# Performance work log

Measured on AMD Instinct MI355X. Metric: run time of the kernel, lower is better.

## Reference

```python
import jax, jax.numpy as jnp
import numpy as np

B, N, D = 16, 2048, 64

def setup_inputs() -> dict:
    key = jax.random.key(0)
    kq, kk, kv = jax.random.split(key, 3)
    q = jax.random.normal(kq, (B, N, D), dtype=jnp.float32)
    k = jax.random.normal(kk, (B, N, D), dtype=jnp.float32)
    v = jax.random.normal(kv, (B, N, D), dtype=jnp.float32)
    scale = jnp.float32(1.0 / np.sqrt(D))  # canonical 1/sqrt(d_head)
    return {"q": q, "k": k, "v": v, "scale": scale}

def reference(q, k, v, scale):
    # attention = softmax((q @ k^T) * scale) over key axis; dropout p=0.0 is identity
    scores = jnp.einsum('bqd,bkd->bqk', q, k) * scale  # [B,N,N]
    attention = jax.nn.softmax(scores, axis=2)
    context = jnp.einsum('bqk,bkd->bqd', attention, v)  # [B,N,D]
    return (context, attention)
```

## Files before the change

### kernel.cpp

```cpp
#include <hip/hip_runtime.h>

#define Bb 16
#define Nn 2048
#define Dd 64

typedef __attribute__((ext_vector_type(8))) short s16x8;
typedef __attribute__((ext_vector_type(4))) short s16x4;
typedef __attribute__((ext_vector_type(4))) float fx4;

__device__ __forceinline__ unsigned short f2bf(float f) {
  union { float f; unsigned u; } v; v.f = f;
  unsigned r = v.u + 0x7FFFu + ((v.u >> 16) & 1u);
  return (unsigned short)(r >> 16);
}

__global__ void k_cvtK(const float* __restrict__ K, unsigned short* __restrict__ Kb) {
  int i = blockIdx.x * 256 + threadIdx.x;
  float4 f = ((const float4*)K)[i];
  ushort4 o;
  o.x = f2bf(f.x); o.y = f2bf(f.y); o.z = f2bf(f.z); o.w = f2bf(f.w);
  ((ushort4*)Kb)[i] = o;
}

__global__ void k_transV(const float* __restrict__ V, unsigned short* __restrict__ VT) {
  __shared__ float tile[32][33];
  int b = blockIdx.z;
  int j0 = blockIdx.x * 32, d0 = blockIdx.y * 32;
  int tx = threadIdx.x, ty = threadIdx.y;
  const float* Vb = V + (size_t)b * Nn * Dd;
  unsigned short* Tb = VT + (size_t)b * Dd * Nn;
  for (int r = ty; r < 32; r += 8)
    tile[r][tx] = Vb[(size_t)(j0 + r) * Dd + d0 + tx];
  __syncthreads();
  for (int r = ty; r < 32; r += 8)
    Tb[(size_t)(d0 + r) * Nn + j0 + tx] = f2bf(tile[tx][r]);
}

__global__ __launch_bounds__(256) void k_attn(
    const float* __restrict__ Q, const unsigned short* __restrict__ Kbf,
    const unsigned short* __restrict__ VTbf, const float* __restrict__ scale_p,
    float* __restrict__ ctx, float* att) {
  const int id = blockIdx.x;
  const int swz = ((id & 7) << 8) | (id >> 3);
  const int b = swz >> 7;
  const int q0 = (swz & 127) << 4;

  const int tid = threadIdx.x;
  const int wave = tid >> 6, lane = tid & 63;
  const int nl = lane & 15, quad = lane >> 4;
  const int qrow = q0 + nl;
  const float c2 = scale_p[0] * 1.44269504088896341f;

  __shared__ float sm[4][16];
  __shared__ float sl[4][16];
  __shared__ float ob[4][16][64];

  s16x8 qb[2];
  {
    const float* qp = Q + ((size_t)b * Nn + qrow) * Dd + quad * 8;
#pragma unroll
    for (int kt = 0; kt < 2; ++kt) {
      float4 f0 = *(const float4*)(qp + kt * 32);
      float4 f1 = *(const float4*)(qp + kt * 32 + 4);
      s16x8 t;
      t[0] = (short)f2bf(f0.x); t[1] = (short)f2bf(f0.y);
      t[2] = (short)f2bf(f0.z); t[3] = (short)f2bf(f0.w);
      t[4] = (short)f2bf(f1.x); t[5] = (short)f2bf(f1.y);
      t[6] = (short)f2bf(f1.z); t[7] = (short)f2bf(f1.w);
      qb[kt] = t;
    }
  }
  const unsigned short* Kb = Kbf + (size_t)b * Nn * Dd;
  const unsigned short* VTb = VTbf + (size_t)b * Dd * Nn;
  float* attb = att + (size_t)b * Nn * Nn;

  float m = -3.0e38f, l = 0.0f;

  for (int t = 0; t < 4; ++t) {
    const int k0 = (wave * 4 + t) * 128;
    fx4 s[8];
#pragma unroll
    for (int nt = 0; nt < 8; ++nt) s[nt] = (fx4){0.f, 0.f, 0.f, 0.f};
#pragma unroll
    for (int nt = 0; nt < 8; ++nt) {
      const s16x8* ka =
          (const s16x8*)(Kb + ((size_t)(k0 + nt * 16 + nl)) * Dd + quad * 8);
      s[nt] = __builtin_amdgcn_mfma_f32_16x16x32_bf16(ka[0], qb[0], s[nt], 0, 0, 0);
      s[nt] = __builtin_amdgcn_mfma_f32_16x16x32_bf16(ka[4], qb[1], s[nt], 0, 0, 0);
    }
    float lm = s[0][0];
#pragma unroll
    for (int nt = 0; nt < 8; ++nt)
#pragma unroll
      for (int r = 0; r < 4; ++r) lm = fmaxf(lm, s[nt][r]);
    float mn = fmaxf(m, lm * c2);
    float ls = 0.f;
#pragma unroll
    for (int nt = 0; nt < 8; ++nt)
#pragma unroll
      for (int r = 0; r < 4; ++r) ls += exp2f(fmaf(s[nt][r], c2, -mn));
    l = l * exp2f(m - mn) + ls;
    m = mn;
  }
#pragma unroll
  for (int mask = 16; mask <= 32; mask <<= 1) {
    float om = __shfl_xor(m, mask, 64);
    float ol = __shfl_xor(l, mask, 64);
    float mn = fmaxf(m, om);
    l = l * exp2f(m - mn) + ol * exp2f(om - mn);
    m = mn;
  }
  if (lane < 16) { sm[wave][lane] = m; sl[wave][lane] = l; }
  __syncthreads();
  float rinv;
  {
    float M = sm[0][nl], L = sl[0][nl];
#pragma unroll
    for (int j = 1; j < 4; ++j) {
      float mj = sm[j][nl], lj = sl[j][nl];
      float mn = fmaxf(M, mj);
      L = L * exp2f(M - mn) + lj * exp2f(mj - mn);
      M = mn;
    }
    m = M;
    rinv = 1.0f / L;
  }

  fx4 o[4];
#pragma unroll
  for (int d = 0; d < 4; ++d) o[d] = (fx4){0.f, 0.f, 0.f, 0.f};

  for (int t = 0; t < 4; ++t) {
    const int k0 = (wave * 4 + t) * 128;
    fx4 s[8];
#pragma unroll
    for (int nt = 0; nt < 8; ++nt) s[nt] = (fx4){0.f, 0.f, 0.f, 0.f};
#pragma unroll
    for (int nt = 0; nt < 8; ++nt) {
      const s16x8* ka =
          (const s16x8*)(Kb + ((size_t)(k0 + nt * 16 + nl)) * Dd + quad * 8);
      s[nt] = __builtin_amdgcn_mfma_f32_16x16x32_bf16(ka[0], qb[0], s[nt], 0, 0, 0);
      s[nt] = __builtin_amdgcn_mfma_f32_16x16x32_bf16(ka[4], qb[1], s[nt], 0, 0, 0);
    }
#pragma unroll
    for (int nt = 0; nt < 8; ++nt) {
      s16x4 vb[4];
#pragma unroll
      for (int ntd = 0; ntd < 4; ++ntd)
        vb[ntd] = *(const s16x4*)(VTb + ((size_t)(ntd * 16 + nl)) * Nn + k0 +
                                  nt * 16 + quad * 4);
      fx4 p;
#pragma unroll
      for (int r = 0; r < 4; ++r)
        p[r] = exp2f(fmaf(s[nt][r], c2, -m)) * rinv;
      *(fx4*)(attb + (size_t)qrow * Nn + k0 + nt * 16 + quad * 4) = p;
      s16x4 pa;
      pa[0] = (short)f2bf(p[0]); pa[1] = (short)f2bf(p[1]);
      pa[2] = (short)f2bf(p[2]); pa[3] = (short)f2bf(p[3]);
#pragma unroll
      for (int ntd = 0; ntd < 4; ++ntd)
        o[ntd] = __builtin_amdgcn_mfma_f32_16x16x16bf16_1k(pa, vb[ntd], o[ntd], 0, 0, 0);
    }
  }

#pragma unroll
  for (int ntd = 0; ntd < 4; ++ntd)
#pragma unroll
    for (int r = 0; r < 4; ++r)
      ob[wave][quad * 4 + r][ntd * 16 + nl] = o[ntd][r];
  __syncthreads();
  {
    const int row = tid >> 4;
    const int col = (tid & 15) << 2;
    fx4 a = *(const fx4*)&ob[0][row][col];
#pragma unroll
    for (int j = 1; j < 4; ++j) {
      fx4 tt = *(const fx4*)&ob[j][row][col];
      a[0] += tt[0]; a[1] += tt[1]; a[2] += tt[2]; a[3] += tt[3];
    }
    *(fx4*)(ctx + ((size_t)b * Nn + q0 + row) * Dd + col) = a;
  }
}

extern "C" void kernel_launch(void* const* d_in, const int* in_sizes, int n_in,
                              void* d_out, int out_size, void* d_ws, size_t ws_size,
                              hipStream_t stream) {
  const float* q = (const float*)d_in[0];
  const float* k = (const float*)d_in[1];
  const float* v = (const float*)d_in[2];
  const float* scale = (const float*)d_in[3];

  float* ctx = (float*)d_out;
  float* att = ctx + (size_t)Bb * Nn * Dd;

  unsigned short* Kbf = (unsigned short*)d_ws;
  unsigned short* VTbf = Kbf + (size_t)Bb * Nn * Dd;

  hipLaunchKernelGGL(k_cvtK, dim3((Bb * Nn * Dd) / (256 * 4)), dim3(256), 0, stream,
                     k, Kbf);
  hipLaunchKernelGGL(k_transV, dim3(Nn / 32, Dd / 32, Bb), dim3(32, 8), 0, stream,
                     v, VTbf);
  hipLaunchKernelGGL(k_attn, dim3(Bb * Nn / 16), dim3(256), 0, stream,
                     q, Kbf, VTbf, scale, ctx, att);
}
```

Before: 493.1 us.

## Stage attention tiles in swizzled LDS for coalesced nontemporal stores; split reductions

The attention probabilities were written straight from the MFMA register layout, so each lane stored 16 bytes at scattered rows. Each wave now stages 16x64 tiles in a per-wave, XOR-swizzled shared buffer and writes whole row segments with nontemporal stores, which should improve coalescing and cut cache pollution on the dominant 268MB output. The row max and sum reductions are also split into four independent chains to shorten dependency latency. This adds LDS traffic and relies on an lgkmcnt wait rather than a barrier within each wave.

```diff
diff --git a/kernel.cpp b/kernel.cpp
--- a/kernel.cpp
+++ b/kernel.cpp
@@ -53,7 +53,7 @@
 
   __shared__ float sm[4][16];
   __shared__ float sl[4][16];
-  __shared__ float ob[4][16][64];
+  __shared__ float obf[4 * 1024];
 
   s16x8 qb[2];
   {
@@ -88,17 +88,23 @@
       s[nt] = __builtin_amdgcn_mfma_f32_16x16x32_bf16(ka[0], qb[0], s[nt], 0, 0, 0);
       s[nt] = __builtin_amdgcn_mfma_f32_16x16x32_bf16(ka[4], qb[1], s[nt], 0, 0, 0);
     }
-    float lm = s[0][0];
-#pragma unroll
-    for (int nt = 0; nt < 8; ++nt)
-#pragma unroll
-      for (int r = 0; r < 4; ++r) lm = fmaxf(lm, s[nt][r]);
+    float x0 = s[0][0], x1 = s[0][1], x2 = s[0][2], x3 = s[0][3];
+#pragma unroll
+    for (int nt = 1; nt < 8; ++nt) {
+      x0 = fmaxf(x0, s[nt][0]); x1 = fmaxf(x1, s[nt][1]);
+      x2 = fmaxf(x2, s[nt][2]); x3 = fmaxf(x3, s[nt][3]);
+    }
+    float lm = fmaxf(fmaxf(x0, x1), fmaxf(x2, x3));
     float mn = fmaxf(m, lm * c2);
-    float ls = 0.f;
-#pragma unroll
-    for (int nt = 0; nt < 8; ++nt)
-#pragma unroll
-      for (int r = 0; r < 4; ++r) ls += exp2f(fmaf(s[nt][r], c2, -mn));
+    float a0 = 0.f, a1 = 0.f, a2 = 0.f, a3 = 0.f;
+#pragma unroll
+    for (int nt = 0; nt < 8; ++nt) {
+      a0 += exp2f(fmaf(s[nt][0], c2, -mn));
+      a1 += exp2f(fmaf(s[nt][1], c2, -mn));
+      a2 += exp2f(fmaf(s[nt][2], c2, -mn));
+      a3 += exp2f(fmaf(s[nt][3], c2, -mn));
+    }
+    float ls = (a0 + a1) + (a2 + a3);
     l = l * exp2f(m - mn) + ls;
     m = mn;
   }
@@ -130,6 +136,8 @@
 #pragma unroll
   for (int d = 0; d < 4; ++d) o[d] = (fx4){0.f, 0.f, 0.f, 0.f};
 
+  float* myob = obf + wave * 1024;
+
   for (int t = 0; t < 4; ++t) {
     const int k0 = (wave * 4 + t) * 128;
     fx4 s[8];
@@ -143,42 +151,66 @@
       s[nt] = __builtin_amdgcn_mfma_f32_16x16x32_bf16(ka[4], qb[1], s[nt], 0, 0, 0);
     }
 #pragma unroll
-    for (int nt = 0; nt < 8; ++nt) {
-      s16x4 vb[4];
-#pragma unroll
-      for (int ntd = 0; ntd < 4; ++ntd)
-        vb[ntd] = *(const s16x4*)(VTb + ((size_t)(ntd * 16 + nl)) * Nn + k0 +
-                                  nt * 16 + quad * 4);
-      fx4 p;
-#pragma unroll
-      for (int r = 0; r < 4; ++r)
-        p[r] = exp2f(fmaf(s[nt][r], c2, -m)) * rinv;
-      *(fx4*)(attb + (size_t)qrow * Nn + k0 + nt * 16 + quad * 4) = p;
-      s16x4 pa;
-      pa[0] = (short)f2bf(p[0]); pa[1] = (short)f2bf(p[1]);
-      pa[2] = (short)f2bf(p[2]); pa[3] = (short)f2bf(p[3]);
-#pragma unroll
-      for (int ntd = 0; ntd < 4; ++ntd)
-        o[ntd] = __builtin_amdgcn_mfma_f32_16x16x16bf16_1k(pa, vb[ntd], o[ntd], 0, 0, 0);
+    for (int c = 0; c < 2; ++c) {
+#pragma unroll
+      for (int n4 = 0; n4 < 4; ++n4) {
+        const int nt = c * 4 + n4;
+        s16x4 vb[4];
+#pragma unroll
+        for (int ntd = 0; ntd < 4; ++ntd)
+          vb[ntd] = *(const s16x4*)(VTb + ((size_t)(ntd * 16 + nl)) * Nn + k0 +
+                                    nt * 16 + quad * 4);
+        fx4 p;
+#pragma unroll
+        for (int r = 0; r < 4; ++r)
+          p[r] = exp2f(fmaf(s[nt][r], c2, -m)) * rinv;
+        {
+          const int su = (n4 * 4 + quad) ^ (nl & 7);
+          *(fx4*)&myob[nl * 64 + su * 4] = p;
+        }
+        s16x4 pa;
+        pa[0] = (short)f2bf(p[0]); pa[1] = (short)f2bf(p[1]);
+        pa[2] = (short)f2bf(p[2]); pa[3] = (short)f2bf(p[3]);
+#pragma unroll
+        for (int ntd = 0; ntd < 4; ++ntd)
+          o[ntd] = __builtin_amdgcn_mfma_f32_16x16x16bf16_1k(pa, vb[ntd], o[ntd], 0, 0, 0);
+      }
+      asm volatile("s_waitcnt lgkmcnt(0)" ::: "memory");
+      {
+        const int rl = lane >> 4, un = lane & 15;
+#pragma unroll
+        for (int rb = 0; rb < 4; ++rb) {
+          const int row = rb * 4 + rl;
+          const int su = un ^ (row & 7);
+          fx4 val = *(const fx4*)&myob[row * 64 + su * 4];
+          __builtin_nontemporal_store(
+              val, (fx4*)(attb + (size_t)(q0 + row) * Nn + k0 + c * 64 + un * 4));
+        }
+      }
     }
   }
 
 #pragma unroll
   for (int ntd = 0; ntd < 4; ++ntd)
 #pragma unroll
-    for (int r = 0; r < 4; ++r)
-      ob[wave][quad * 4 + r][ntd * 16 + nl] = o[ntd][r];
+    for (int r = 0; r < 4; ++r) {
+      const int row = quad * 4 + r;
+      const int unit = ntd * 4 + (nl >> 2);
+      const int su = unit ^ (row & 7);
+      myob[row * 64 + su * 4 + (nl & 3)] = o[ntd][r];
+    }
   __syncthreads();
   {
     const int row = tid >> 4;
-    const int col = (tid & 15) << 2;
-    fx4 a = *(const fx4*)&ob[0][row][col];
+    const int un = tid & 15;
+    const int su = un ^ (row & 7);
+    fx4 a = *(const fx4*)&obf[row * 64 + su * 4];
 #pragma unroll
     for (int j = 1; j < 4; ++j) {
-      fx4 tt = *(const fx4*)&ob[j][row][col];
+      fx4 tt = *(const fx4*)&obf[j * 1024 + row * 64 + su * 4];
       a[0] += tt[0]; a[1] += tt[1]; a[2] += tt[2]; a[3] += tt[3];
     }
-    *(fx4*)(ctx + ((size_t)b * Nn + q0 + row) * Dd + col) = a;
+    *(fx4*)(ctx + ((size_t)b * Nn + q0 + row) * Dd + un * 4) = a;
   }
 }
 
```

Measured after the change: 491.2 us. Within noise of the previous version (-0.4%).
